# Kernel tuning notes

Measured on AMD Instinct MI355X. Metric: run time of the kernel, lower is better.

Reference implementation:

```python
import jax, jax.numpy as jnp
import numpy as np

IN_F = 11008   # named 'in_features' in the module but used as the OUTPUT dim of F.linear
OUT_F = 4096   # named 'out_features' but is x's feature (input) dim
GROUP = 64


def dequantize_q40(w, s):
    """w: int8 (IN_F*OUT_F/GROUP/2, GROUP) packed nibbles; s: fp16 (IN_F*OUT_F/GROUP,).
    Matches torch: MSB = w >> 4 (arithmetic), LSB = w << 4 >> 4 (sign-extended low nibble).
    """
    msb = (w >> 4).astype(jnp.float16)                      # arithmetic shift on int8
    lsb = ((w & 15) - ((w & 8) << 1)).astype(jnp.float16)   # sign-extend low 4 bits to [-8, 7]
    q = jnp.concatenate([msb, lsb], axis=1).reshape(-1, GROUP)  # (n_groups, GROUP)
    fpval = (q * s[:, None]).astype(jnp.float16)
    return fpval.reshape(IN_F, OUT_F)


def setup_inputs() -> dict:
    key = jax.random.key(0)
    k1, k2, k3 = jax.random.split(key, 3)
    x = jax.random.normal(k1, (4, 2048, OUT_F), dtype=jnp.float16)
    n_rows = IN_F * OUT_F // GROUP // 2
    w = jax.random.randint(k2, (n_rows, GROUP), -128, 128, dtype=jnp.int32).astype(jnp.int8)
    s = (jax.random.uniform(k3, (IN_F * OUT_F // GROUP,), dtype=jnp.float32) * 0.02 + 0.001).astype(jnp.float16)
    return {"x": x, "w": w, "s": s}


def reference(x, w, s):
    # F.linear(x, deq) with deq of shape (IN_F, OUT_F): y = x @ deq.T
    deq = dequantize_q40(w, s)  # (IN_F, OUT_F) fp16
    return jnp.einsum('bsk,ok->bso', x, deq)  # (4, 2048, IN_F)
```

## Files before the change

kernel.cpp:

```cpp
#include <hip/hip_runtime.h>
#include <stdint.h>

#define M_DIM 8192
#define K_DIM 4096
#define N_DIM 11008

#define BM 128
#define BN 128
#define BK 64


typedef __attribute__((ext_vector_type(8))) _Float16 half8;
typedef __attribute__((ext_vector_type(4))) _Float16 half4;
typedef __attribute__((ext_vector_type(4))) float floatx4;

#define SWZ(row, col) ((col) ^ (((row) & 7) << 3))

#define GLD_LDS16(gp, lp)                                                     \
    __builtin_amdgcn_global_load_lds(                                         \
        (const __attribute__((address_space(1))) uint32_t*)(gp),              \
        (__attribute__((address_space(3))) uint32_t*)(lp), 16, 0, 0)

__global__ __launch_bounds__(256) void dequant_q40(const int* __restrict__ w,
                                                   const float* __restrict__ s,
                                                   _Float16* __restrict__ deq) {
    int t = blockIdx.x * 256 + threadIdx.x;
    int r = t >> 3;
    int j = (t & 7) * 8;
    const int* wp = w + (size_t)r * 64 + j;
    int4 p0 = *(const int4*)(wp);
    int4 p1 = *(const int4*)(wp + 4);
    float sm = s[2 * r];
    float sl = s[2 * r + 1];
    int n = r >> 5, u = r & 31;
    _Float16* dm = deq + (size_t)n * K_DIM + u * 128 + j;
    int v[8] = {p0.x, p0.y, p0.z, p0.w, p1.x, p1.y, p1.z, p1.w};
    half8 vm, vl;
#pragma unroll
    for (int i = 0; i < 8; ++i) {
        int b = v[i];
        vm[i] = (_Float16)((float)(b >> 4) * sm);
        vl[i] = (_Float16)((float)((b << 28) >> 28) * sl);
    }
    *(half8*)dm = vm;
    *(half8*)(dm + 64) = vl;
}

__global__ __launch_bounds__(256) void conv_a16(const float* __restrict__ A,
                                                _Float16* __restrict__ A16) {
    size_t t = (size_t)blockIdx.x * 256 + threadIdx.x;
    const float* p = A + t * 8;
    float4 v0 = *(const float4*)(p);
    float4 v1 = *(const float4*)(p + 4);
    half8 h;
    h[0] = (_Float16)v0.x; h[1] = (_Float16)v0.y;
    h[2] = (_Float16)v0.z; h[3] = (_Float16)v0.w;
    h[4] = (_Float16)v1.x; h[5] = (_Float16)v1.y;
    h[6] = (_Float16)v1.z; h[7] = (_Float16)v1.w;
    *(half8*)(A16 + t * 8) = h;
}

__global__ __launch_bounds__(256, 2) void gemm_lds16(const _Float16* __restrict__ A,
                                                     const _Float16* __restrict__ B,
                                                     float* __restrict__ C) {
    __shared__ _Float16 As[BM * BK];
    __shared__ _Float16 Bs[BN * BK];

    const int tid  = threadIdx.x;
    const int lane = tid & 63;
    const int wave = tid >> 6;
    const int wm = (wave >> 1) * 64;
    const int wn = (wave & 1) * 64;

    const int nwg_per_xcd = (N_DIM / BN) * (M_DIM / BM) / 8;
    int bid = blockIdx.x;
    int swz = (bid & 7) * nwg_per_xcd + (bid >> 3);
    const int n0 = (swz % (N_DIM / BN)) * BN;
    const int m0 = (swz / (N_DIM / BN)) * BM;

    const int lrow8 = lane >> 3;
    const int lcol  = ((lane & 7) * 8) ^ (lrow8 << 3);

    const _Float16* aptr = A + (size_t)(m0 + wave * 32 + lrow8) * K_DIM + lcol;
    const _Float16* bptr = B + (size_t)(n0 + wave * 32 + lrow8) * K_DIM + lcol;
    _Float16* asl = As + (wave * 32) * BK;
    _Float16* bsl = Bs + (wave * 32) * BK;

    floatx4 acc[4][4] = {};
    const int lrow = lane & 15;
    const int quad = lane >> 4;
    const int kxor = (lrow & 7) << 3;

    for (int kk = 0; kk < K_DIM; kk += BK) {
        __syncthreads();
#pragma unroll
        for (int i = 0; i < 4; ++i)
            GLD_LDS16(aptr + (size_t)(i * 8) * K_DIM + kk, asl + i * 8 * BK);
#pragma unroll
        for (int i = 0; i < 4; ++i)
            GLD_LDS16(bptr + (size_t)(i * 8) * K_DIM + kk, bsl + i * 8 * BK);
        __syncthreads();

#pragma unroll
        for (int ks = 0; ks < BK; ks += 32) {
            int koff = (ks + quad * 8) ^ kxor;
            half8 af[4], bf[4];
#pragma unroll
            for (int im = 0; im < 4; ++im)
                af[im] = *(const half8*)(As + (wm + im * 16 + lrow) * BK + koff);
#pragma unroll
            for (int in_ = 0; in_ < 4; ++in_)
                bf[in_] = *(const half8*)(Bs + (wn + in_ * 16 + lrow) * BK + koff);
#pragma unroll
            for (int im = 0; im < 4; ++im)
#pragma unroll
                for (int in_ = 0; in_ < 4; ++in_)
                    acc[im][in_] = __builtin_amdgcn_mfma_f32_16x16x32_f16(
                        af[im], bf[in_], acc[im][in_], 0, 0, 0);
        }
    }

#pragma unroll
    for (int im = 0; im < 4; ++im) {
#pragma unroll
        for (int in_ = 0; in_ < 4; ++in_) {
            int col = n0 + wn + in_ * 16 + lrow;
#pragma unroll
            for (int r = 0; r < 4; ++r) {
                int row = m0 + wm + im * 16 + quad * 4 + r;
                C[(size_t)row * N_DIM + col] = acc[im][in_][r];
            }
        }
    }
}

__global__ __launch_bounds__(256, 2) void gemm_f16_bt(const float* __restrict__ A,
                                                      const _Float16* __restrict__ B,
                                                      float* __restrict__ C) {
    __shared__ _Float16 As[BM * BK];
    __shared__ _Float16 Bs[BN * BK];

    const int tid  = threadIdx.x;
    const int lane = tid & 63;
    const int wave = tid >> 6;
    const int wm = (wave >> 1) * 64;
    const int wn = (wave & 1) * 64;
    const int m0 = blockIdx.y * BM;
    const int n0 = blockIdx.x * BN;

    floatx4 acc[4][4] = {};
    const int lrow = lane & 15;
    const int quad = lane >> 4;
    const int kxor = (lrow & 7) << 3;

    for (int kk = 0; kk < K_DIM; kk += BK) {
        float4 av[8];
#pragma unroll
        for (int i = 0; i < 8; ++i) {
            int flat = i * 256 + tid;
            int row = flat >> 4;
            int col = (flat & 15) * 4;
            av[i] = *(const float4*)(A + (size_t)(m0 + row) * K_DIM + kk + col);
        }
        half8 bv[4];
#pragma unroll
        for (int i = 0; i < 4; ++i) {
            int flat = i * 256 + tid;
            int row = flat >> 3;
            int col = (flat & 7) * 8;
            bv[i] = *(const half8*)(B + (size_t)(n0 + row) * K_DIM + kk + col);
        }
        __syncthreads();
#pragma unroll
        for (int i = 0; i < 8; ++i) {
            int flat = i * 256 + tid;
            int row = flat >> 4;
            int col = (flat & 15) * 4;
            half4 a16;
            a16[0] = (_Float16)av[i].x;
            a16[1] = (_Float16)av[i].y;
            a16[2] = (_Float16)av[i].z;
            a16[3] = (_Float16)av[i].w;
            *(half4*)(As + row * BK + SWZ(row, col)) = a16;
        }
#pragma unroll
        for (int i = 0; i < 4; ++i) {
            int flat = i * 256 + tid;
            int row = flat >> 3;
            int col = (flat & 7) * 8;
            *(half8*)(Bs + row * BK + SWZ(row, col)) = bv[i];
        }
        __syncthreads();

#pragma unroll
        for (int ks = 0; ks < BK; ks += 32) {
            int koff = (ks + quad * 8) ^ kxor;
            half8 af[4], bf[4];
#pragma unroll
            for (int im = 0; im < 4; ++im)
                af[im] = *(const half8*)(As + (wm + im * 16 + lrow) * BK + koff);
#pragma unroll
            for (int in_ = 0; in_ < 4; ++in_)
                bf[in_] = *(const half8*)(Bs + (wn + in_ * 16 + lrow) * BK + koff);
#pragma unroll
            for (int im = 0; im < 4; ++im)
#pragma unroll
                for (int in_ = 0; in_ < 4; ++in_)
                    acc[im][in_] = __builtin_amdgcn_mfma_f32_16x16x32_f16(
                        af[im], bf[in_], acc[im][in_], 0, 0, 0);
        }
    }

#pragma unroll
    for (int im = 0; im < 4; ++im) {
#pragma unroll
        for (int in_ = 0; in_ < 4; ++in_) {
            int col = n0 + wn + in_ * 16 + lrow;
#pragma unroll
            for (int r = 0; r < 4; ++r) {
                int row = m0 + wm + im * 16 + quad * 4 + r;
                C[(size_t)row * N_DIM + col] = acc[im][in_][r];
            }
        }
    }
}

__global__ __launch_bounds__(256, 2) void gemm_fused(const float* __restrict__ A,
                                                     const int* __restrict__ W,
                                                     const float* __restrict__ S,
                                                     float* __restrict__ C) {
    __shared__ _Float16 As[BM * BK];
    __shared__ _Float16 Bs[BN * BK];

    const int tid  = threadIdx.x;
    const int lane = tid & 63;
    const int wave = tid >> 6;
    const int wm = (wave >> 1) * 64;
    const int wn = (wave & 1) * 64;
    const int m0 = blockIdx.y * BM;
    const int n0 = blockIdx.x * BN;

    floatx4 acc[4][4] = {};
    const int lrow = lane & 15;
    const int quad = lane >> 4;
    const int kxor = (lrow & 7) << 3;

    const int nn = tid >> 1;
    const int bh = (tid & 1) * 32;

    for (int kk = 0; kk < K_DIM; kk += BK) {
        float4 av[8];
#pragma unroll
        for (int i = 0; i < 8; ++i) {
            int flat = i * 256 + tid;
            int row = flat >> 4;
            int col = (flat & 15) * 4;
            av[i] = *(const float4*)(A + (size_t)(m0 + row) * K_DIM + kk + col);
        }
        int t64 = kk >> 6;
        int u = t64 >> 1;
        const int* wr = W + ((size_t)(n0 + nn) * 32 + u) * 64 + bh;
        float sc = S[(size_t)(n0 + nn) * 64 + t64];
        bool sel_lsb = (t64 & 1);
        half8 bq[4];
#pragma unroll
        for (int i8 = 0; i8 < 4; ++i8) {
            int4 pa = *(const int4*)(wr + i8 * 8);
            int4 pb = *(const int4*)(wr + i8 * 8 + 4);
            int vv[8] = {pa.x, pa.y, pa.z, pa.w, pb.x, pb.y, pb.z, pb.w};
#pragma unroll
            for (int q = 0; q < 8; ++q) {
                int b = vv[q];
                int qq = sel_lsb ? ((b << 28) >> 28) : (b >> 4);
                bq[i8][q] = (_Float16)((float)qq * sc);
            }
        }
        __syncthreads();
#pragma unroll
        for (int i = 0; i < 8; ++i) {
            int flat = i * 256 + tid;
            int row = flat >> 4;
            int col = (flat & 15) * 4;
            half4 a16;
            a16[0] = (_Float16)av[i].x;
            a16[1] = (_Float16)av[i].y;
            a16[2] = (_Float16)av[i].z;
            a16[3] = (_Float16)av[i].w;
            *(half4*)(As + row * BK + SWZ(row, col)) = a16;
        }
#pragma unroll
        for (int i8 = 0; i8 < 4; ++i8)
            *(half8*)(Bs + nn * BK + SWZ(nn, bh + i8 * 8)) = bq[i8];
        __syncthreads();

#pragma unroll
        for (int ks = 0; ks < BK; ks += 32) {
            int koff = (ks + quad * 8) ^ kxor;
            half8 af[4], bf[4];
#pragma unroll
            for (int im = 0; im < 4; ++im)
                af[im] = *(const half8*)(As + (wm + im * 16 + lrow) * BK + koff);
#pragma unroll
            for (int in_ = 0; in_ < 4; ++in_)
                bf[in_] = *(const half8*)(Bs + (wn + in_ * 16 + lrow) * BK + koff);
#pragma unroll
            for (int im = 0; im < 4; ++im)
#pragma unroll
                for (int in_ = 0; in_ < 4; ++in_)
                    acc[im][in_] = __builtin_amdgcn_mfma_f32_16x16x32_f16(
                        af[im], bf[in_], acc[im][in_], 0, 0, 0);
        }
    }

#pragma unroll
    for (int im = 0; im < 4; ++im) {
#pragma unroll
        for (int in_ = 0; in_ < 4; ++in_) {
            int col = n0 + wn + in_ * 16 + lrow;
#pragma unroll
            for (int r = 0; r < 4; ++r) {
                int row = m0 + wm + im * 16 + quad * 4 + r;
                C[(size_t)row * N_DIM + col] = acc[im][in_][r];
            }
        }
    }
}

extern "C" void kernel_launch(void* const* d_in, const int* in_sizes, int n_in,
                              void* d_out, int out_size, void* d_ws, size_t ws_size,
                              hipStream_t stream) {
    const float* x = (const float*)d_in[0];
    const int*   w = (const int*)d_in[1];
    const float* s = (const float*)d_in[2];
    float*     out = (float*)d_out;

    const size_t deq_bytes = (size_t)N_DIM * K_DIM * sizeof(_Float16);
    const size_t a16_bytes = (size_t)M_DIM * K_DIM * sizeof(_Float16);

    if (ws_size >= deq_bytes + a16_bytes) {
        _Float16* deq = (_Float16*)d_ws;
        _Float16* a16 = (_Float16*)((char*)d_ws + deq_bytes);
        dequant_q40<<<11008, 256, 0, stream>>>(w, s, deq);
        conv_a16<<<(M_DIM * K_DIM / 8) / 256, 256, 0, stream>>>(x, a16);
        gemm_lds16<<<(N_DIM / BN) * (M_DIM / BM), 256, 0, stream>>>(a16, deq, out);
    } else if (ws_size >= deq_bytes) {
        _Float16* deq = (_Float16*)d_ws;
        dim3 grid(N_DIM / BN, M_DIM / BM);
        dequant_q40<<<11008, 256, 0, stream>>>(w, s, deq);
        gemm_f16_bt<<<grid, 256, 0, stream>>>(x, deq, out);
    } else {
        dim3 grid(N_DIM / BN, M_DIM / BM);
        gemm_fused<<<grid, 256, 0, stream>>>(x, w, s, out);
    }
}
```

Measured before the change: 1.324 ms.

## Replace GEMM with 256x256 double-buffered 8-wave phased pipeline kernel

Replaces the 128x128 single-buffered GEMM with a 256x256 tile kernel using 512 threads, double-buffered LDS, and an explicitly phased schedule. Global-to-LDS loads for the next K tile are interleaved with MFMA work on the current tile, using manual barriers, waitcnt, and setprio. The aim is to hide memory latency and raise arithmetic intensity per tile. Risks include 128KB of LDS per block limiting occupancy, higher register pressure from 32 accumulators, and a wave-quantization tail since 43x32 tiles do not divide evenly across CUs.

```diff
diff --git a/kernel.cpp b/kernel.cpp
--- a/kernel.cpp
+++ b/kernel.cpp
@@ -4,6 +4,12 @@
 #define M_DIM 8192
 #define K_DIM 4096
 #define N_DIM 11008
+
+#define BM2 256
+#define BN2 256
+#define BK2 64
+#define TILE_H (256 * 64)
+#define NT (K_DIM / BK2)
 
 #define BM 128
 #define BN 128
@@ -60,75 +66,126 @@
     *(half8*)(A16 + t * 8) = h;
 }
 
-__global__ __launch_bounds__(256, 2) void gemm_lds16(const _Float16* __restrict__ A,
-                                                     const _Float16* __restrict__ B,
-                                                     float* __restrict__ C) {
-    __shared__ _Float16 As[BM * BK];
-    __shared__ _Float16 Bs[BN * BK];
+__global__ __launch_bounds__(512, 2) void gemm_8ph(const _Float16* __restrict__ A,
+                                                   const _Float16* __restrict__ B,
+                                                   float* __restrict__ C) {
+    __shared__ _Float16 As[2 * TILE_H];
+    __shared__ _Float16 Bs[2 * TILE_H];
 
     const int tid  = threadIdx.x;
     const int lane = tid & 63;
     const int wave = tid >> 6;
-    const int wm = (wave >> 1) * 64;
-    const int wn = (wave & 1) * 64;
-
-    const int nwg_per_xcd = (N_DIM / BN) * (M_DIM / BM) / 8;
+    const int wr = wave >> 2;
+    const int wc = wave & 3;
+
     int bid = blockIdx.x;
-    int swz = (bid & 7) * nwg_per_xcd + (bid >> 3);
-    const int n0 = (swz % (N_DIM / BN)) * BN;
-    const int m0 = (swz / (N_DIM / BN)) * BM;
-
-    const int lrow8 = lane >> 3;
-    const int lcol  = ((lane & 7) * 8) ^ (lrow8 << 3);
-
-    const _Float16* aptr = A + (size_t)(m0 + wave * 32 + lrow8) * K_DIM + lcol;
-    const _Float16* bptr = B + (size_t)(n0 + wave * 32 + lrow8) * K_DIM + lcol;
-    _Float16* asl = As + (wave * 32) * BK;
-    _Float16* bsl = Bs + (wave * 32) * BK;
-
-    floatx4 acc[4][4] = {};
+    int swz = (bid & 7) * 172 + (bid >> 3);
+    const int n0 = (swz % 43) * BN2;
+    const int m0 = (swz / 43) * BM2;
+
+    const int srow = lane >> 3;
+    const int scol = ((lane & 7) * 8) ^ (srow << 3);
+    const _Float16* aptr = A + (size_t)(m0 + wave * 8 + srow) * K_DIM + scol;
+    const _Float16* bptr = B + (size_t)(n0 + wave * 8 + srow) * K_DIM + scol;
+
+#define STAGE_A8(cbn, c, kof) \
+    GLD_LDS16(aptr + (size_t)((c) * 64) * K_DIM + (kof), &As[(cbn) + (c) * 4096 + wave * 512])
+#define STAGE_B8(cbn, c, kof) \
+    GLD_LDS16(bptr + (size_t)((c) * 64) * K_DIM + (kof), &Bs[(cbn) + (c) * 4096 + wave * 512])
+
+    floatx4 acc[8][4] = {};
+    half8 af[4], bf[4];
     const int lrow = lane & 15;
     const int quad = lane >> 4;
     const int kxor = (lrow & 7) << 3;
-
-    for (int kk = 0; kk < K_DIM; kk += BK) {
-        __syncthreads();
-#pragma unroll
-        for (int i = 0; i < 4; ++i)
-            GLD_LDS16(aptr + (size_t)(i * 8) * K_DIM + kk, asl + i * 8 * BK);
-#pragma unroll
-        for (int i = 0; i < 4; ++i)
-            GLD_LDS16(bptr + (size_t)(i * 8) * K_DIM + kk, bsl + i * 8 * BK);
-        __syncthreads();
-
-#pragma unroll
-        for (int ks = 0; ks < BK; ks += 32) {
-            int koff = (ks + quad * 8) ^ kxor;
-            half8 af[4], bf[4];
-#pragma unroll
-            for (int im = 0; im < 4; ++im)
-                af[im] = *(const half8*)(As + (wm + im * 16 + lrow) * BK + koff);
-#pragma unroll
-            for (int in_ = 0; in_ < 4; ++in_)
-                bf[in_] = *(const half8*)(Bs + (wn + in_ * 16 + lrow) * BK + koff);
-#pragma unroll
-            for (int im = 0; im < 4; ++im)
-#pragma unroll
-                for (int in_ = 0; in_ < 4; ++in_)
-                    acc[im][in_] = __builtin_amdgcn_mfma_f32_16x16x32_f16(
-                        af[im], bf[in_], acc[im][in_], 0, 0, 0);
-        }
-    }
-
-#pragma unroll
-    for (int im = 0; im < 4; ++im) {
+    const int arow = wr * 128 + lrow;
+    const int brow = wc * 64 + lrow;
+
+#define DS_A4(cb, mh, ks)                                                      \
+    {                                                                          \
+        const int kq = ((ks) * 32 + quad * 8) ^ kxor;                          \
+        af[0] = *(const half8*)&As[(cb) + (arow + (mh) * 64 +  0) * 64 + kq];  \
+        af[1] = *(const half8*)&As[(cb) + (arow + (mh) * 64 + 16) * 64 + kq];  \
+        af[2] = *(const half8*)&As[(cb) + (arow + (mh) * 64 + 32) * 64 + kq];  \
+        af[3] = *(const half8*)&As[(cb) + (arow + (mh) * 64 + 48) * 64 + kq];  \
+    }
+#define DS_B4(cb, ks)                                                          \
+    {                                                                          \
+        const int kq = ((ks) * 32 + quad * 8) ^ kxor;                          \
+        bf[0] = *(const half8*)&Bs[(cb) + (brow +  0) * 64 + kq];              \
+        bf[1] = *(const half8*)&Bs[(cb) + (brow + 16) * 64 + kq];              \
+        bf[2] = *(const half8*)&Bs[(cb) + (brow + 32) * 64 + kq];              \
+        bf[3] = *(const half8*)&Bs[(cb) + (brow + 48) * 64 + kq];              \
+    }
+#define MFMA16(mh)                                                             \
+    _Pragma("unroll")                                                          \
+    for (int im = 0; im < 4; ++im)                                             \
+        _Pragma("unroll")                                                      \
+        for (int in_ = 0; in_ < 4; ++in_)                                      \
+            acc[(mh) * 4 + im][in_] = __builtin_amdgcn_mfma_f32_16x16x32_f16(  \
+                af[im], bf[in_], acc[(mh) * 4 + im][in_], 0, 0, 0);
+
+#define BAR   asm volatile("s_barrier" ::: "memory")
+#define WAITL asm volatile("s_waitcnt lgkmcnt(0)" ::: "memory");               \
+              __builtin_amdgcn_sched_barrier(0)
+#define WVM2  asm volatile("s_waitcnt vmcnt(2)" ::: "memory");                 \
+              __builtin_amdgcn_sched_barrier(0)
+#define WVM0  asm volatile("s_waitcnt vmcnt(0)" ::: "memory");                 \
+              __builtin_amdgcn_sched_barrier(0)
+#define PRIO1 __builtin_amdgcn_s_setprio(1)
+#define PRIO0 __builtin_amdgcn_s_setprio(0)
+
+    STAGE_B8(0, 0, 0); STAGE_B8(0, 1, 0); STAGE_B8(0, 2, 0); STAGE_B8(0, 3, 0);
+    STAGE_A8(0, 0, 0); STAGE_A8(0, 2, 0); STAGE_A8(0, 1, 0); STAGE_A8(0, 3, 0);
+    WVM2;
+    BAR;
+
+    int cb = 0;
+    for (int t = 0; t < NT - 1; ++t) {
+        const int cbn = cb ^ TILE_H;
+        const size_t kof = (size_t)(t + 1) * BK2;
+        DS_A4(cb, 0, 0); DS_B4(cb, 0);
+        STAGE_B8(cbn, 0, kof); STAGE_B8(cbn, 1, kof);
+        BAR; WAITL;
+        PRIO1; MFMA16(0); PRIO0;
+        WVM2; BAR;
+        DS_A4(cb, 1, 0);
+        STAGE_B8(cbn, 2, kof); STAGE_B8(cbn, 3, kof);
+        BAR; WAITL;
+        PRIO1; MFMA16(1); PRIO0;
+        BAR;
+        DS_A4(cb, 0, 1); DS_B4(cb, 1);
+        STAGE_A8(cbn, 0, kof); STAGE_A8(cbn, 2, kof);
+        BAR; WAITL;
+        PRIO1; MFMA16(0); PRIO0;
+        BAR;
+        DS_A4(cb, 1, 1);
+        STAGE_A8(cbn, 1, kof); STAGE_A8(cbn, 3, kof);
+        BAR; WAITL;
+        PRIO1; MFMA16(1); PRIO0;
+        WVM2; BAR;
+        cb = cbn;
+    }
+
+    DS_A4(cb, 0, 0); DS_B4(cb, 0);
+    WAITL; PRIO1; MFMA16(0); PRIO0;
+    WVM0; BAR;
+    DS_A4(cb, 1, 0);
+    WAITL; PRIO1; MFMA16(1); PRIO0;
+    DS_A4(cb, 0, 1); DS_B4(cb, 1);
+    WAITL; PRIO1; MFMA16(0); PRIO0;
+    DS_A4(cb, 1, 1);
+    WAITL; PRIO1; MFMA16(1); PRIO0;
+
+#pragma unroll
+    for (int mf = 0; mf < 8; ++mf) {
 #pragma unroll
         for (int in_ = 0; in_ < 4; ++in_) {
-            int col = n0 + wn + in_ * 16 + lrow;
+            int col = n0 + wc * 64 + in_ * 16 + lrow;
 #pragma unroll
             for (int r = 0; r < 4; ++r) {
-                int row = m0 + wm + im * 16 + quad * 4 + r;
-                C[(size_t)row * N_DIM + col] = acc[im][in_][r];
+                int row = m0 + wr * 128 + mf * 16 + quad * 4 + r;
+                C[(size_t)row * N_DIM + col] = acc[mf][in_][r];
             }
         }
     }
@@ -342,7 +399,7 @@
         _Float16* a16 = (_Float16*)((char*)d_ws + deq_bytes);
         dequant_q40<<<11008, 256, 0, stream>>>(w, s, deq);
         conv_a16<<<(M_DIM * K_DIM / 8) / 256, 256, 0, stream>>>(x, a16);
-        gemm_lds16<<<(N_DIM / BN) * (M_DIM / BM), 256, 0, stream>>>(a16, deq, out);
+        gemm_8ph<<<(M_DIM / BM2) * (N_DIM / BN2), 512, 0, stream>>>(a16, deq, out);
     } else if (ws_size >= deq_bytes) {
         _Float16* deq = (_Float16*)d_ws;
         dim3 grid(N_DIM / BN, M_DIM / BM);
```

Result: no change. 1.305 ms (-1.4%).
